# Kernel optimization log

Measured on AMD Instinct MI355X. Metric: run time of the kernel, lower is better.

The kernel has to match this reference:

```python
import jax, jax.numpy as jnp
import numpy as np

N = 50000      # nodes
E = 800000     # edges (avg degree 16)
IN = 256       # input feature dim
HID = 128      # hidden dim
H = 4          # heads
C = HID // H   # per-head dim = 32
L = 3          # layers


def setup_inputs() -> dict:
    key = jax.random.key(0)
    ks = jax.random.split(key, 16)
    s = 0.02
    f32 = jnp.float32
    inp = {
        "x": jax.random.normal(ks[0], (N, IN), f32),
        "edge_index": jax.random.randint(ks[1], (2, E), 0, N, dtype=jnp.int32),
        "edge_attr": jax.random.normal(ks[2], (E, 1), f32),
        "Wi": jax.random.normal(ks[3], (IN, HID), f32) * s,
        "bi": jnp.zeros((HID,), f32),
        "Wq": jax.random.normal(ks[4], (L, HID, HID), f32) * s,
        "bq": jnp.zeros((L, HID), f32),
        "Wk": jax.random.normal(ks[5], (L, HID, HID), f32) * s,
        "bk": jnp.zeros((L, HID), f32),
        "Wv": jax.random.normal(ks[6], (L, HID, HID), f32) * s,
        "bv": jnp.zeros((L, HID), f32),
        "We": jax.random.normal(ks[7], (L, 1, HID), f32) * s,      # lin_edge, no bias
        "Wskip": jax.random.normal(ks[8], (L, HID, HID), f32) * s,
        "bskip": jnp.zeros((L, HID), f32),
        "Wbeta": jax.random.normal(ks[9], (L, 3 * HID, 1), f32) * s,  # lin_beta, no bias
        "ln_g": jnp.ones((L, HID), f32),
        "ln_b": jnp.zeros((L, HID), f32),
    }
    return inp


def _layer_norm(x, g, b, eps=1e-5):
    mu = jnp.mean(x, axis=-1, keepdims=True)
    var = jnp.var(x, axis=-1, keepdims=True)
    return (x - mu) * jax.lax.rsqrt(var + eps) * g + b


def _transformer_conv(h, src, dst, edge_attr, Wq, bq, Wk, bk, Wv, bv, We, Wskip, bskip, Wbeta):
    # node-level projections [N, HID]
    q = h @ Wq + bq
    k = h @ Wk + bk
    v = h @ Wv + bv
    e = edge_attr @ We                       # [E, HID] edge embedding
    # per-edge gathered features [E, H, C]
    qi = q[dst].reshape(E, H, C)
    kj = (k[src] + e).reshape(E, H, C)
    vj = (v[src] + e).reshape(E, H, C)
    # attention logits [E, H]
    alpha = jnp.sum(qi * kj, axis=-1) / np.sqrt(C)
    # segment softmax over destination node
    amax = jax.ops.segment_max(alpha, dst, num_segments=N)   # [N, H]
    ex = jnp.exp(alpha - amax[dst])
    denom = jax.ops.segment_sum(ex, dst, num_segments=N)     # [N, H]
    attn = ex / (denom[dst] + 1e-16)                         # [E, H]
    # scatter-add aggregation -> [N, H, C] -> concat heads [N, HID]
    out = jax.ops.segment_sum(attn[..., None] * vj, dst, num_segments=N).reshape(N, HID)
    # gated skip (beta=True, root_weight=True)
    x_r = h @ Wskip + bskip
    beta = jax.nn.sigmoid(jnp.concatenate([out, x_r, out - x_r], axis=-1) @ Wbeta)  # [N, 1]
    return beta * x_r + (1.0 - beta) * out


def reference(x, edge_index, edge_attr, Wi, bi, Wq, bq, Wk, bk, Wv, bv, We, Wskip, bskip, Wbeta, ln_g, ln_b):
    src = edge_index[0]
    dst = edge_index[1]
    h = x @ Wi + bi
    for l in range(L):
        res = h
        h = _transformer_conv(h, src, dst, edge_attr,
                              Wq[l], bq[l], Wk[l], bk[l], Wv[l], bv[l],
                              We[l], Wskip[l], bskip[l], Wbeta[l])
        h = jax.nn.gelu(h, approximate=False)
        h = _layer_norm(h + res, ln_g[l], ln_b[l])
        # dropout: eval mode -> identity
    return h
```

## Files before the change

### kernel.cpp

```cpp
#include <hip/hip_runtime.h>
#include <math.h>

#define NNODES 50000
#define NEDGES 800000
#define DIN 256
#define DHID 128
#define GBLK 391
#define QBLK 782
#define NBUCK 196
#define CHUNK 4096

typedef __attribute__((ext_vector_type(8))) short short8;
typedef __attribute__((ext_vector_type(4))) float f32x4;
typedef __attribute__((ext_vector_type(2))) float f32x2;

__device__ __forceinline__ unsigned short f2bf(float f) {
    unsigned u = __builtin_bit_cast(unsigned, f);
    u += 0x7fffu + ((u >> 16) & 1u);
    return (unsigned short)(u >> 16);
}
__device__ __forceinline__ float bf2f(unsigned short s) {
    return __builtin_bit_cast(float, (unsigned)s << 16);
}
__device__ __forceinline__ unsigned packbf(float a, float b) {
    return (unsigned)f2bf(a) | ((unsigned)f2bf(b) << 16);
}
__device__ __forceinline__ float dpp_xor1(float x) {
    return __builtin_bit_cast(float, __builtin_amdgcn_update_dpp(0, __builtin_bit_cast(int, x), 0xB1, 0xF, 0xF, true));
}
__device__ __forceinline__ float dpp_xor2(float x) {
    return __builtin_bit_cast(float, __builtin_amdgcn_update_dpp(0, __builtin_bit_cast(int, x), 0x4E, 0xF, 0xF, true));
}
__device__ __forceinline__ float dpp_hmirror(float x) {
    return __builtin_bit_cast(float, __builtin_amdgcn_update_dpp(0, __builtin_bit_cast(int, x), 0x141, 0xF, 0xF, true));
}
__device__ __forceinline__ float dpp_mirror(float x) {
    return __builtin_bit_cast(float, __builtin_amdgcn_update_dpp(0, __builtin_bit_cast(int, x), 0x140, 0xF, 0xF, true));
}
__device__ __forceinline__ float red16(float x) {
    x += dpp_xor1(x);
    x += dpp_xor2(x);
    x += dpp_hmirror(x);
    x += dpp_mirror(x);
    return x;
}

__global__ __launch_bounds__(256) void prep_hist(const float* __restrict__ Wi, const float* __restrict__ Wq,
                                                 const float* __restrict__ Wk, const float* __restrict__ Wv,
                                                 const float* __restrict__ Ws, unsigned short* __restrict__ Wit,
                                                 unsigned short* __restrict__ Wt3, const int* __restrict__ dst,
                                                 int* __restrict__ counts, int pb) {
    if ((int)blockIdx.x < pb) {
        int idx = blockIdx.x * 256 + threadIdx.x;
        if (idx < DHID * DIN) {
            int n = idx >> 8, kk = idx & 255;
            Wit[idx] = f2bf(Wi[kk * DHID + n]);
        }
        int idx2 = idx - DHID * DIN;
        if (idx2 >= 0 && idx2 < 3 * 512 * DHID) {
            int l = idx2 / (512 * DHID);
            int rem = idx2 - l * 512 * DHID;
            int r = rem >> 7;
            int kk = rem & 127;
            int sel = r >> 7, rl = r & 127;
            const float* srcm = sel == 0 ? Wq : sel == 1 ? Wk : sel == 2 ? Wv : Ws;
            Wt3[idx2] = f2bf(srcm[l * DHID * DHID + kk * DHID + rl]);
        }
    } else {
        int e = (blockIdx.x - pb) * 256 + threadIdx.x;
        if (e < NEDGES) atomicAdd(&counts[dst[e]], 1);
    }
}

__global__ __launch_bounds__(256) void k_scan_block(const int* __restrict__ in, int* __restrict__ out,
                                                    int* __restrict__ partials, int n, int* __restrict__ dh) {
    __shared__ int sh[256];
    __shared__ int dhist[256];
    int tid = threadIdx.x;
    int i = blockIdx.x * 256 + tid;
    int vv = (i < n) ? in[i] : 0;
    sh[tid] = vv;
    dhist[tid] = 0;
    __syncthreads();
    if (i < n) atomicAdd(&dhist[min(vv, 255)], 1);
    for (int off = 1; off < 256; off <<= 1) {
        int t = (tid >= off) ? sh[tid - off] : 0;
        __syncthreads();
        sh[tid] += t;
        __syncthreads();
    }
    if (i < n) out[i] = sh[tid];
    if (tid == 255) partials[blockIdx.x] = sh[255];
    __syncthreads();
    int hc = dhist[tid];
    if (hc) atomicAdd(&dh[tid], hc);
}

__global__ __launch_bounds__(256) void k_apply2(const int* __restrict__ partials, int* __restrict__ row_ptr, int n,
                                                int nb, const int* __restrict__ dh, int* __restrict__ dbase) {
    __shared__ int sh[256];
    int tid = threadIdx.x;
    int vv = (tid < nb) ? partials[tid] : 0;
    sh[tid] = vv;
    __syncthreads();
    for (int off = 1; off < 256; off <<= 1) {
        int t = (tid >= off) ? sh[tid - off] : 0;
        __syncthreads();
        sh[tid] += t;
        __syncthreads();
    }
    int i = blockIdx.x * 256 + tid;
    if (i < n) {
        int add = blockIdx.x ? sh[blockIdx.x - 1] : 0;
        row_ptr[i + 1] += add;
    }
    if (i == 0) row_ptr[0] = 0;
    if (blockIdx.x == 0) {
        __syncthreads();
        int c = dh[255 - tid];
        sh[tid] = c;
        __syncthreads();
        for (int off = 1; off < 256; off <<= 1) {
            int t = (tid >= off) ? sh[tid - off] : 0;
            __syncthreads();
            sh[tid] += t;
            __syncthreads();
        }
        dbase[255 - tid] = sh[tid] - c;
    }
}

__global__ __launch_bounds__(256) void perm_scatter(const int* __restrict__ counts, const int* __restrict__ dbase,
                                                    int* __restrict__ dfill, int* __restrict__ perm) {
    __shared__ int h[256], gb[256], c2[256];
    const int tid = threadIdx.x;
    int i = blockIdx.x * 256 + tid;
    int d = (i < NNODES) ? min(counts[i], 255) : -1;
    h[tid] = 0;
    c2[tid] = 0;
    __syncthreads();
    if (d >= 0) atomicAdd(&h[d], 1);
    __syncthreads();
    int c = h[tid];
    gb[tid] = c ? dbase[tid] + atomicAdd(&dfill[tid], c) : 0;
    __syncthreads();
    if (d >= 0) {
        int r = atomicAdd(&c2[d], 1);
        perm[gb[d] + r] = i;
    }
}

__global__ __launch_bounds__(256) void bin_edges(const int* __restrict__ src, const int* __restrict__ dst,
                                                 const float* __restrict__ ea, const int* __restrict__ row_ptr,
                                                 int* __restrict__ bfill, unsigned* __restrict__ brec,
                                                 unsigned char* __restrict__ bdst) {
    __shared__ int hist[NBUCK];
    __shared__ int lbase[NBUCK];
    __shared__ int gbase[NBUCK];
    __shared__ int cnt[NBUCK];
    __shared__ unsigned rec4[CHUNK];
    __shared__ unsigned char dl8[CHUNK];
    __shared__ unsigned char bk8[CHUNK];
    const int tid = threadIdx.x;
    const int e0 = blockIdx.x * CHUNK;
    const int n = min(NEDGES - e0, CHUNK);
    for (int i = tid; i < NBUCK; i += 256) hist[i] = 0;
    __syncthreads();
    for (int i = tid; i < n; i += 256) atomicAdd(&hist[dst[e0 + i] >> 8], 1);
    __syncthreads();
    if (tid == 0) {
        int run = 0;
        for (int b = 0; b < NBUCK; ++b) {
            lbase[b] = run;
            run += hist[b];
        }
    }
    __syncthreads();
    for (int b = tid; b < NBUCK; b += 256) {
        int h = hist[b];
        int off = h ? atomicAdd(&bfill[b], h) : 0;
        gbase[b] = row_ptr[b << 8] + off;
        cnt[b] = lbase[b];
    }
    __syncthreads();
    for (int i = tid; i < n; i += 256) {
        int d = dst[e0 + i];
        int b = d >> 8;
        int lp = atomicAdd(&cnt[b], 1);
        rec4[lp] = (unsigned)src[e0 + i] | ((unsigned)f2bf(ea[e0 + i]) << 16);
        dl8[lp] = (unsigned char)(d & 255);
        bk8[lp] = (unsigned char)b;
    }
    __syncthreads();
    for (int i = tid; i < n; i += 256) {
        int b = bk8[i];
        int pos = gbase[b] + (i - lbase[b]);
        brec[pos] = rec4[i];
        bdst[pos] = dl8[i];
    }
}

__global__ __launch_bounds__(256) void sort_bucket(const unsigned* __restrict__ brec,
                                                   const unsigned char* __restrict__ bdst,
                                                   const int* __restrict__ row_ptr, unsigned* __restrict__ esrc) {
    __shared__ int rp[257];
    __shared__ int cnt[256];
    const int b = blockIdx.x;
    const int d0 = b << 8;
    const int nmax = min(256, NNODES - d0);
    const int tid = threadIdx.x;
    for (int i = tid; i <= nmax; i += 256) rp[i] = row_ptr[d0 + i];
    cnt[tid] = 0;
    __syncthreads();
    const int base = rp[0], end = rp[nmax];
    for (int i = base + tid; i < end; i += 256) {
        unsigned rec = brec[i];
        int d = bdst[i];
        int rank = atomicAdd(&cnt[d], 1);
        esrc[rp[d] + rank] = rec;
    }
}

__global__ __launch_bounds__(256) void gemm_in(const float* __restrict__ A, const unsigned short* __restrict__ Wt,
                                               const float* __restrict__ bias, unsigned* __restrict__ h32, int M) {
    __shared__ short As[128 * 128];
    const int tid = threadIdx.x;
    const int lane = tid & 63;
    const int wid = tid >> 6;
    const int row0 = blockIdx.x * 128;
    const int wr = (wid & 1) * 64;
    const int wc = (wid >> 1) * 64;
    f32x4 acc[4][4] = {};
    const int srow = tid >> 1;
    const int sk = (tid & 1) * 64;
    const int grow = min(row0 + srow, M - 1);
    for (int kt = 0; kt < 2; ++kt) {
        const float* ap = A + (size_t)grow * DIN + kt * 128 + sk;
#pragma unroll
        for (int i = 0; i < 8; ++i) {
            float4 f0 = *(const float4*)(ap + i * 8);
            float4 f1 = *(const float4*)(ap + i * 8 + 4);
            short8 s;
            s[0] = f2bf(f0.x); s[1] = f2bf(f0.y); s[2] = f2bf(f0.z); s[3] = f2bf(f0.w);
            s[4] = f2bf(f1.x); s[5] = f2bf(f1.y); s[6] = f2bf(f1.z); s[7] = f2bf(f1.w);
            int g = (sk >> 3) + i;
            *(short8*)(&As[srow * 128 + ((g ^ (srow & 7)) << 3)]) = s;
        }
        __syncthreads();
#pragma unroll
        for (int ks = 0; ks < 4; ++ks) {
            short8 a[4], b[4];
#pragma unroll
            for (int m = 0; m < 4; ++m) {
                int r = wr + m * 16 + (lane & 15);
                int g = ks * 4 + (lane >> 4);
                a[m] = *(const short8*)(&As[r * 128 + ((g ^ (r & 7)) << 3)]);
            }
#pragma unroll
            for (int n = 0; n < 4; ++n) {
                int c = wc + n * 16 + (lane & 15);
                b[n] = *(const short8*)(Wt + (size_t)c * DIN + kt * 128 + ks * 32 + (lane >> 4) * 8);
            }
#pragma unroll
            for (int m = 0; m < 4; ++m)
#pragma unroll
                for (int n = 0; n < 4; ++n)
                    acc[m][n] = __builtin_amdgcn_mfma_f32_16x16x32_bf16(a[m], b[n], acc[m][n], 0, 0, 0);
        }
        __syncthreads();
    }
    float* my = ((float*)As) + wid * 1024;
    float bb[4];
#pragma unroll
    for (int n = 0; n < 4; ++n) bb[n] = bias[wc + n * 16 + (lane & 15)];
    const int rr = lane >> 2;
    const int cb = lane & 3;
#pragma unroll
    for (int m = 0; m < 4; ++m) {
#pragma unroll
        for (int n = 0; n < 4; ++n) {
            int lc = n * 16 + (lane & 15);
#pragma unroll
            for (int j = 0; j < 4; ++j) {
                int row = (lane >> 4) * 4 + j;
                my[row * 64 + (((lc >> 2) ^ (row & 7)) << 2) + (lc & 3)] = acc[m][n][j] + bb[n];
            }
        }
        float vals[16];
#pragma unroll
        for (int s = 0; s < 4; ++s) {
            int gx = (cb * 4 + s) ^ (rr & 7);
            f32x4 t4 = *(const f32x4*)(my + rr * 64 + gx * 4);
            vals[s * 4 + 0] = t4.x; vals[s * 4 + 1] = t4.y; vals[s * 4 + 2] = t4.z; vals[s * 4 + 3] = t4.w;
        }
        int grow2 = row0 + wr + m * 16 + rr;
        if (grow2 < M) {
            unsigned pk[8];
#pragma unroll
            for (int d = 0; d < 8; ++d) pk[d] = packbf(vals[2 * d], vals[2 * d + 1]);
            unsigned* op = h32 + (size_t)grow2 * 64 + (wc >> 1) + cb * 8;
            *(uint4*)op = make_uint4(pk[0], pk[1], pk[2], pk[3]);
            *(uint4*)(op + 4) = make_uint4(pk[4], pk[5], pk[6], pk[7]);
        }
    }
}

__global__ __launch_bounds__(256) void gemm_qkvs(const unsigned short* __restrict__ A,
                                                 const unsigned short* __restrict__ Wt, const float* __restrict__ bq,
                                                 const float* __restrict__ bk, const float* __restrict__ bv,
                                                 const float* __restrict__ bs, unsigned* __restrict__ q32,
                                                 unsigned* __restrict__ kv, unsigned* __restrict__ xr32, int M) {
    __shared__ short As[64 * 128];
    const int tid = threadIdx.x;
    const int lane = tid & 63;
    const int wid = tid >> 6;
    const int row0 = blockIdx.x * 64;
    const int sel = wid >> 1;
    const int wc = (wid & 1) * 64;
    f32x4 acc0[4][4] = {}, acc1[4][4] = {};
    {
        const int srow = tid >> 2;
        const int sk = (tid & 3) * 32;
        const int grow = min(row0 + srow, M - 1);
        const unsigned short* ap = A + (size_t)grow * DHID + sk;
#pragma unroll
        for (int i = 0; i < 4; ++i) {
            short8 s = *(const short8*)(ap + i * 8);
            int g = (sk >> 3) + i;
            *(short8*)(&As[srow * 128 + ((g ^ (srow & 7)) << 3)]) = s;
        }
    }
    __syncthreads();
    const int b0base = sel ? 128 : 0;
    const int b1base = sel ? 256 : 384;
#pragma unroll
    for (int ks = 0; ks < 4; ++ks) {
        short8 a[4], b0[4], b1[4];
#pragma unroll
        for (int m = 0; m < 4; ++m) {
            int r = m * 16 + (lane & 15);
            int g = ks * 4 + (lane >> 4);
            a[m] = *(const short8*)(&As[r * 128 + ((g ^ (r & 7)) << 3)]);
        }
#pragma unroll
        for (int n = 0; n < 4; ++n) {
            int rb = wc + n * 16 + (lane & 15);
            b0[n] = *(const short8*)(Wt + (size_t)(b0base + rb) * DHID + ks * 32 + (lane >> 4) * 8);
            b1[n] = *(const short8*)(Wt + (size_t)(b1base + rb) * DHID + ks * 32 + (lane >> 4) * 8);
        }
#pragma unroll
        for (int m = 0; m < 4; ++m)
#pragma unroll
            for (int n = 0; n < 4; ++n) {
                acc0[m][n] = __builtin_amdgcn_mfma_f32_16x16x32_bf16(a[m], b0[n], acc0[m][n], 0, 0, 0);
                acc1[m][n] = __builtin_amdgcn_mfma_f32_16x16x32_bf16(a[m], b1[n], acc1[m][n], 0, 0, 0);
            }
    }
    __syncthreads();
    float* my = ((float*)As) + wid * 1024;
    const float* bias0 = sel ? bk : bq;
    const float* bias1 = sel ? bv : bs;
    float bb0[4], bb1[4];
#pragma unroll
    for (int n = 0; n < 4; ++n) {
        int c = wc + n * 16 + (lane & 15);
        bb0[n] = bias0[c];
        bb1[n] = bias1[c];
    }
    const int rr = lane >> 2;
    const int cb = lane & 3;
#pragma unroll
    for (int m = 0; m < 4; ++m) {
        float vals0[16], vals1[16];
#pragma unroll
        for (int n = 0; n < 4; ++n) {
            int lc = n * 16 + (lane & 15);
#pragma unroll
            for (int j = 0; j < 4; ++j) {
                int row = (lane >> 4) * 4 + j;
                my[row * 64 + (((lc >> 2) ^ (row & 7)) << 2) + (lc & 3)] = acc0[m][n][j] + bb0[n];
            }
        }
#pragma unroll
        for (int s = 0; s < 4; ++s) {
            int gx = (cb * 4 + s) ^ (rr & 7);
            f32x4 t4 = *(const f32x4*)(my + rr * 64 + gx * 4);
            vals0[s * 4 + 0] = t4.x; vals0[s * 4 + 1] = t4.y; vals0[s * 4 + 2] = t4.z; vals0[s * 4 + 3] = t4.w;
        }
#pragma unroll
        for (int n = 0; n < 4; ++n) {
            int lc = n * 16 + (lane & 15);
#pragma unroll
            for (int j = 0; j < 4; ++j) {
                int row = (lane >> 4) * 4 + j;
                my[row * 64 + (((lc >> 2) ^ (row & 7)) << 2) + (lc & 3)] = acc1[m][n][j] + bb1[n];
            }
        }
#pragma unroll
        for (int s = 0; s < 4; ++s) {
            int gx = (cb * 4 + s) ^ (rr & 7);
            f32x4 t4 = *(const f32x4*)(my + rr * 64 + gx * 4);
            vals1[s * 4 + 0] = t4.x; vals1[s * 4 + 1] = t4.y; vals1[s * 4 + 2] = t4.z; vals1[s * 4 + 3] = t4.w;
        }
        int grow2 = row0 + m * 16 + rr;
        if (grow2 < M) {
            size_t obase = (size_t)grow2 * 64 + (wc >> 1) + cb * 8;
            if (sel == 0) {
                unsigned p0[8], p1[8];
#pragma unroll
                for (int d = 0; d < 8; ++d) {
                    p0[d] = packbf(vals0[2 * d], vals0[2 * d + 1]);
                    p1[d] = packbf(vals1[2 * d], vals1[2 * d + 1]);
                }
                *(uint4*)(q32 + obase) = make_uint4(p0[0], p0[1], p0[2], p0[3]);
                *(uint4*)(q32 + obase + 4) = make_uint4(p0[4], p0[5], p0[6], p0[7]);
                *(uint4*)(xr32 + obase) = make_uint4(p1[0], p1[1], p1[2], p1[3]);
                *(uint4*)(xr32 + obase + 4) = make_uint4(p1[4], p1[5], p1[6], p1[7]);
            } else {
                unsigned pk[8];
#pragma unroll
                for (int d = 0; d < 8; ++d) {
                    unsigned u = (unsigned)__builtin_amdgcn_cvt_pk_fp8_f32(vals0[2 * d], vals0[2 * d + 1], 0, false);
                    u = (unsigned)__builtin_amdgcn_cvt_pk_fp8_f32(vals1[2 * d], vals1[2 * d + 1], (int)u, true);
                    pk[d] = u;
                }
                *(uint4*)(kv + obase) = make_uint4(pk[0], pk[1], pk[2], pk[3]);
                *(uint4*)(kv + obase + 4) = make_uint4(pk[4], pk[5], pk[6], pk[7]);
            }
        }
    }
}

__global__ __launch_bounds__(256) void node_attn_fuse(const unsigned* __restrict__ q32,
                                                      const unsigned* __restrict__ kv, const unsigned* __restrict__ esrc,
                                                      const float* __restrict__ We, const int* __restrict__ row_ptr,
                                                      const int* __restrict__ perm, const unsigned* __restrict__ xr32,
                                                      const unsigned* res32, const float* __restrict__ Wb,
                                                      const float* __restrict__ lng, const float* __restrict__ lnb,
                                                      unsigned* houtb, float* houtf) {
    const int tid = threadIdx.x;
    const int lane = tid & 63;
    const int lnl = lane & 15;
    const int gbase = lane & 48;
    const int node = perm[blockIdx.x * 16 + (tid >> 4)];
    const int base = row_ptr[node], end = row_ptr[node + 1];
    const float SC = 0.25505654047688565f;
    const float THR = 8.0f;

    float qv[8], wev[8];
    {
        uint4 qw = *(const uint4*)(q32 + (size_t)node * 64 + 4 * lnl);
        unsigned qd[4] = {qw.x, qw.y, qw.z, qw.w};
#pragma unroll
        for (int t = 0; t < 4; ++t) {
            qv[2 * t] = bf2f((unsigned short)qd[t]) * SC;
            qv[2 * t + 1] = bf2f((unsigned short)(qd[t] >> 16)) * SC;
        }
        float4 wlo = *(const float4*)(We + 8 * lnl);
        float4 whi = *(const float4*)(We + 8 * lnl + 4);
        wev[0] = wlo.x; wev[1] = wlo.y; wev[2] = wlo.z; wev[3] = wlo.w;
        wev[4] = whi.x; wev[5] = whi.y; wev[6] = whi.z; wev[7] = whi.w;
    }
    float qwe;
    {
        float s = 0.f;
#pragma unroll
        for (int i = 0; i < 8; ++i) s = fmaf(qv[i], wev[i], s);
        s += dpp_xor1(s);
        s += dpp_xor2(s);
        qwe = s;
    }

    float m = -1e30f, sden = 0.f, tacc = 0.f;
    float acc[8] = {};
    const unsigned* kvp = kv + 4 * lnl;

    for (int off = 0; ; off += 16) {
        int cnt = min(end - base - off, 16);
        if (__all(cnt <= 0)) break;
        unsigned u_l = 0;
        if (lnl < cnt) u_l = esrc[base + off + lnl];
        int cm = max(cnt, 0);
        cm = max(cm, __shfl_xor(cm, 16));
        cm = max(cm, __shfl_xor(cm, 32));
        unsigned ue0 = (unsigned)__shfl((int)u_l, gbase + 0);
        unsigned ue1 = (unsigned)__shfl((int)u_l, gbase + 1);
        unsigned ue2 = (unsigned)__shfl((int)u_l, gbase + 2);
        unsigned ue3 = (unsigned)__shfl((int)u_l, gbase + 3);
        uint4 kw0 = *(const uint4*)(kvp + (size_t)(ue0 & 0xFFFFu) * 64);
        uint4 kw1 = *(const uint4*)(kvp + (size_t)(ue1 & 0xFFFFu) * 64);
        uint4 kw2 = *(const uint4*)(kvp + (size_t)(ue2 & 0xFFFFu) * 64);
        uint4 kw3 = *(const uint4*)(kvp + (size_t)(ue3 & 0xFFFFu) * 64);
        for (int j = 0; j < cm; j += 2) {
            uint4 ka = kw0, kb = kw1;
            unsigned ua = ue0, ub = ue1;
            ue0 = ue2; ue1 = ue3; kw0 = kw2; kw1 = kw3;
            if (j + 4 < cm) {
                ue2 = (unsigned)__shfl((int)u_l, gbase + j + 4);
                ue3 = (unsigned)__shfl((int)u_l, gbase + j + 5);
                kw2 = *(const uint4*)(kvp + (size_t)(ue2 & 0xFFFFu) * 64);
                kw3 = *(const uint4*)(kvp + (size_t)(ue3 & 0xFFFFu) * 64);
            }
            float av0 = bf2f((unsigned short)(ua >> 16));
            float av1 = bf2f((unsigned short)(ub >> 16));
            unsigned kd0[4] = {ka.x, ka.y, ka.z, ka.w};
            unsigned kd1[4] = {kb.x, kb.y, kb.z, kb.w};
            float vj0[8], vj1[8];
            float p0 = 0.f, p1 = 0.f;
#pragma unroll
            for (int t = 0; t < 4; ++t) {
                f32x2 k0 = __builtin_amdgcn_cvt_pk_f32_fp8((int)kd0[t], false);
                f32x2 v0 = __builtin_amdgcn_cvt_pk_f32_fp8((int)kd0[t], true);
                f32x2 k1 = __builtin_amdgcn_cvt_pk_f32_fp8((int)kd1[t], false);
                f32x2 v1 = __builtin_amdgcn_cvt_pk_f32_fp8((int)kd1[t], true);
                p0 = fmaf(qv[2 * t], k0.x, p0);
                p0 = fmaf(qv[2 * t + 1], k0.y, p0);
                p1 = fmaf(qv[2 * t], k1.x, p1);
                p1 = fmaf(qv[2 * t + 1], k1.y, p1);
                vj0[2 * t] = v0.x; vj0[2 * t + 1] = v0.y;
                vj1[2 * t] = v1.x; vj1[2 * t + 1] = v1.y;
            }
            p0 += dpp_xor1(p0);
            p0 += dpp_xor2(p0);
            p1 += dpp_xor1(p1);
            p1 += dpp_xor2(p1);
            p0 = fmaf(av0, qwe, p0);
            p1 = fmaf(av1, qwe, p1);
            p0 = (j < cnt) ? p0 : -3e38f;
            p1 = (j + 1 < cnt) ? p1 : -3e38f;
            float pm = fmaxf(p0, p1);
            if (__any(pm - m > THR)) {
                float mn2 = fmaxf(m, pm);
                float sc = exp2f(m - mn2);
                float w0 = exp2f(p0 - mn2), w1 = exp2f(p1 - mn2);
                sden = fmaf(sden, sc, w0 + w1);
                tacc = fmaf(tacc, sc, fmaf(w0, av0, w1 * av1));
#pragma unroll
                for (int i = 0; i < 8; ++i) acc[i] = fmaf(acc[i], sc, fmaf(w0, vj0[i], w1 * vj1[i]));
                m = mn2;
            } else {
                float w0 = exp2f(p0 - m), w1 = exp2f(p1 - m);
                sden += w0 + w1;
                tacc = fmaf(w0, av0, fmaf(w1, av1, tacc));
#pragma unroll
                for (int i = 0; i < 8; ++i) acc[i] = fmaf(w0, vj0[i], fmaf(w1, vj1[i], acc[i]));
            }
        }
    }

    float rden = 1.f / (sden + 1e-16f);
    float o[8];
#pragma unroll
    for (int i = 0; i < 8; ++i) o[i] = fmaf(tacc, wev[i], acc[i]) * rden;

    float x[8];
    {
        uint4 xw = *(const uint4*)(xr32 + (size_t)node * 64 + 4 * lnl);
        unsigned xd[4] = {xw.x, xw.y, xw.z, xw.w};
#pragma unroll
        for (int t = 0; t < 4; ++t) {
            x[2 * t] = bf2f((unsigned short)xd[t]);
            x[2 * t + 1] = bf2f((unsigned short)(xd[t] >> 16));
        }
    }
    float bl = 0.f;
#pragma unroll
    for (int t = 0; t < 2; ++t) {
        float4 w0 = *(const float4*)(Wb + 8 * lnl + 4 * t);
        float4 w1 = *(const float4*)(Wb + 128 + 8 * lnl + 4 * t);
        float4 w2 = *(const float4*)(Wb + 256 + 8 * lnl + 4 * t);
        bl = fmaf(o[4 * t], w0.x, bl); bl = fmaf(o[4 * t + 1], w0.y, bl);
        bl = fmaf(o[4 * t + 2], w0.z, bl); bl = fmaf(o[4 * t + 3], w0.w, bl);
        bl = fmaf(x[4 * t], w1.x, bl); bl = fmaf(x[4 * t + 1], w1.y, bl);
        bl = fmaf(x[4 * t + 2], w1.z, bl); bl = fmaf(x[4 * t + 3], w1.w, bl);
        bl = fmaf(o[4 * t] - x[4 * t], w2.x, bl); bl = fmaf(o[4 * t + 1] - x[4 * t + 1], w2.y, bl);
        bl = fmaf(o[4 * t + 2] - x[4 * t + 2], w2.z, bl); bl = fmaf(o[4 * t + 3] - x[4 * t + 3], w2.w, bl);
    }
    bl = red16(bl);
    float beta = 1.f / (1.f + __expf(-bl));
    float tpre[8];
    {
        uint4 rw = *(const uint4*)(res32 + (size_t)node * 64 + 4 * lnl);
        unsigned rd[4] = {rw.x, rw.y, rw.z, rw.w};
#pragma unroll
        for (int i = 0; i < 8; ++i) {
            float gg = beta * x[i] + (1.f - beta) * o[i];
            gg = 0.5f * gg * (1.f + erff(gg * 0.70710678118654752f));
            float rv = (i & 1) ? bf2f((unsigned short)(rd[i >> 1] >> 16)) : bf2f((unsigned short)rd[i >> 1]);
            tpre[i] = gg + rv;
        }
    }
    float su = 0.f, sq = 0.f;
#pragma unroll
    for (int i = 0; i < 8; ++i) {
        su += tpre[i];
        sq = fmaf(tpre[i], tpre[i], sq);
    }
    su = red16(su);
    sq = red16(sq);
    float mu = su * (1.f / 128.f);
    float var = sq * (1.f / 128.f) - mu * mu;
    float inv = rsqrtf(var + 1e-5f);
    float4 g0 = *(const float4*)(lng + 8 * lnl);
    float4 g1 = *(const float4*)(lng + 8 * lnl + 4);
    float4 b0 = *(const float4*)(lnb + 8 * lnl);
    float4 b1 = *(const float4*)(lnb + 8 * lnl + 4);
    float gg[8] = {g0.x, g0.y, g0.z, g0.w, g1.x, g1.y, g1.z, g1.w};
    float bb[8] = {b0.x, b0.y, b0.z, b0.w, b1.x, b1.y, b1.z, b1.w};
    float ov[8];
#pragma unroll
    for (int i = 0; i < 8; ++i) ov[i] = (tpre[i] - mu) * inv * gg[i] + bb[i];
    if (houtf) {
        float* op = houtf + (size_t)node * 128 + 8 * lnl;
        *(float4*)op = make_float4(ov[0], ov[1], ov[2], ov[3]);
        *(float4*)(op + 4) = make_float4(ov[4], ov[5], ov[6], ov[7]);
    } else {
        unsigned pk[4];
#pragma unroll
        for (int d = 0; d < 4; ++d) pk[d] = packbf(ov[2 * d], ov[2 * d + 1]);
        *(uint4*)(houtb + (size_t)node * 64 + 4 * lnl) = make_uint4(pk[0], pk[1], pk[2], pk[3]);
    }
}

extern "C" void kernel_launch(void* const* d_in, const int* in_sizes, int n_in, void* d_out, int out_size,
                              void* d_ws, size_t ws_size, hipStream_t stream) {
    const float* x = (const float*)d_in[0];
    const int* ei = (const int*)d_in[1];
    const float* ea = (const float*)d_in[2];
    const float* Wi = (const float*)d_in[3];
    const float* bi = (const float*)d_in[4];
    const float* Wq = (const float*)d_in[5];
    const float* bq = (const float*)d_in[6];
    const float* Wk = (const float*)d_in[7];
    const float* bk = (const float*)d_in[8];
    const float* Wv = (const float*)d_in[9];
    const float* bv = (const float*)d_in[10];
    const float* We = (const float*)d_in[11];
    const float* Wskip = (const float*)d_in[12];
    const float* bskip = (const float*)d_in[13];
    const float* Wbeta = (const float*)d_in[14];
    const float* lng = (const float*)d_in[15];
    const float* lnb = (const float*)d_in[16];

    const int* srcp = ei;
    const int* dstp = ei + NEDGES;

    char* p = (char*)d_ws;
    auto alloc = [&](size_t bytes) {
        void* r = (void*)p;
        p += (bytes + 255) & ~(size_t)255;
        return r;
    };
    unsigned* h32 = (unsigned*)alloc((size_t)NNODES * 64 * 4);
    unsigned* q32 = (unsigned*)alloc((size_t)NNODES * 64 * 4);
    unsigned* xr32 = (unsigned*)alloc((size_t)NNODES * 64 * 4);
    unsigned* kv = (unsigned*)alloc((size_t)NNODES * 64 * 4);
    unsigned short* Wit = (unsigned short*)alloc((size_t)DHID * DIN * 2);
    unsigned short* Wt3 = (unsigned short*)alloc((size_t)3 * 512 * DHID * 2);
    int* counts = (int*)alloc((size_t)(NNODES + 768) * 4);
    int* bfill = counts + NNODES;
    int* dh = bfill + 256;
    int* dfill = dh + 256;
    int* dbase = (int*)alloc(256 * 4);
    int* perm = (int*)alloc((size_t)NNODES * 4);
    int* row_ptr = (int*)alloc((size_t)(NNODES + 1) * 4);
    unsigned* esrc = (unsigned*)alloc((size_t)NEDGES * 4);
    unsigned* brec = (unsigned*)alloc((size_t)NEDGES * 4);
    unsigned char* bdst = (unsigned char*)alloc((size_t)NEDGES);
    int* partials = (int*)alloc(256 * 4);

    const int EB = (NEDGES + 255) / 256;
    const int NB = (NNODES + 255) / 256;
    const int WB = NNODES / 16;
    const int PB = (DHID * DIN + 3 * 512 * DHID + 255) / 256;
    const int AB = (NEDGES + CHUNK - 1) / CHUNK;

    hipMemsetAsync(counts, 0, (size_t)(NNODES + 768) * 4, stream);
    prep_hist<<<PB + EB, 256, 0, stream>>>(Wi, Wq, Wk, Wv, Wskip, Wit, Wt3, dstp, counts, PB);
    gemm_in<<<GBLK, 256, 0, stream>>>(x, Wit, bi, h32, NNODES);
    k_scan_block<<<NB, 256, 0, stream>>>(counts, row_ptr + 1, partials, NNODES, dh);
    k_apply2<<<NB, 256, 0, stream>>>(partials, row_ptr, NNODES, NB, dh, dbase);
    perm_scatter<<<NB, 256, 0, stream>>>(counts, dbase, dfill, perm);
    bin_edges<<<AB, 256, 0, stream>>>(srcp, dstp, ea, row_ptr, bfill, brec, bdst);
    sort_bucket<<<NBUCK, 256, 0, stream>>>(brec, bdst, row_ptr, esrc);

    for (int l = 0; l < 3; ++l) {
        const size_t bo = (size_t)l * 128;
        gemm_qkvs<<<QBLK, 256, 0, stream>>>((const unsigned short*)h32, Wt3 + (size_t)l * 512 * DHID, bq + bo, bk + bo,
                                            bv + bo, bskip + bo, q32, kv, xr32, NNODES);
        node_attn_fuse<<<WB, 256, 0, stream>>>(q32, kv, esrc, We + bo, row_ptr, perm, xr32, h32,
                                               Wbeta + (size_t)l * 384, lng + bo, lnb + bo, h32,
                                               (l == 2) ? (float*)d_out : nullptr);
    }
}
```

Before: 324.2 us.

## Process four edges per step with deeper prefetch; enlarge QKVS GEMM tile

The attention loop now handles four gathered neighbours per iteration and keeps a second batch of four prefetched K/V rows in flight. It also decodes the V halves only when accumulating, which is meant to hide gather latency better and cut loop overhead. The QKV/skip GEMM moves to 128-row tiles with 512 threads, so each block reuses the weight loads across twice as many rows. The cost is higher register pressure in both kernels, a leftover dead conversion loop, and fewer, larger GEMM blocks that may lower occupancy.

New measurement: 311.1 us. -4.1%, faster.

```diff
diff --git a/kernel.cpp b/kernel.cpp
--- a/kernel.cpp
+++ b/kernel.cpp
@@ -6,7 +6,6 @@
 #define DIN 256
 #define DHID 128
 #define GBLK 391
-#define QBLK 782
 #define NBUCK 196
 #define CHUNK 4096
 
@@ -305,18 +304,19 @@
     }
 }
 
-__global__ __launch_bounds__(256) void gemm_qkvs(const unsigned short* __restrict__ A,
+__global__ __launch_bounds__(512) void gemm_qkvs(const unsigned short* __restrict__ A,
                                                  const unsigned short* __restrict__ Wt, const float* __restrict__ bq,
                                                  const float* __restrict__ bk, const float* __restrict__ bv,
                                                  const float* __restrict__ bs, unsigned* __restrict__ q32,
                                                  unsigned* __restrict__ kv, unsigned* __restrict__ xr32, int M) {
-    __shared__ short As[64 * 128];
+    __shared__ short As[128 * 128];
     const int tid = threadIdx.x;
     const int lane = tid & 63;
     const int wid = tid >> 6;
-    const int row0 = blockIdx.x * 64;
-    const int sel = wid >> 1;
-    const int wc = (wid & 1) * 64;
+    const int row0 = blockIdx.x * 128;
+    const int sel = wid >> 2;
+    const int wr = (wid & 1) * 64;
+    const int wc = ((wid >> 1) & 1) * 64;
     f32x4 acc0[4][4] = {}, acc1[4][4] = {};
     {
         const int srow = tid >> 2;
@@ -338,7 +338,7 @@
         short8 a[4], b0[4], b1[4];
 #pragma unroll
         for (int m = 0; m < 4; ++m) {
-            int r = m * 16 + (lane & 15);
+            int r = wr + m * 16 + (lane & 15);
             int g = ks * 4 + (lane >> 4);
             a[m] = *(const short8*)(&As[r * 128 + ((g ^ (r & 7)) << 3)]);
         }
@@ -402,7 +402,7 @@
             f32x4 t4 = *(const f32x4*)(my + rr * 64 + gx * 4);
             vals1[s * 4 + 0] = t4.x; vals1[s * 4 + 1] = t4.y; vals1[s * 4 + 2] = t4.z; vals1[s * 4 + 3] = t4.w;
         }
-        int grow2 = row0 + m * 16 + rr;
+        int grow2 = row0 + wr + m * 16 + rr;
         if (grow2 < M) {
             size_t obase = (size_t)grow2 * 64 + (wc >> 1) + cb * 8;
             if (sel == 0) {
@@ -483,67 +483,96 @@
         int cm = max(cnt, 0);
         cm = max(cm, __shfl_xor(cm, 16));
         cm = max(cm, __shfl_xor(cm, 32));
-        unsigned ue0 = (unsigned)__shfl((int)u_l, gbase + 0);
-        unsigned ue1 = (unsigned)__shfl((int)u_l, gbase + 1);
-        unsigned ue2 = (unsigned)__shfl((int)u_l, gbase + 2);
-        unsigned ue3 = (unsigned)__shfl((int)u_l, gbase + 3);
-        uint4 kw0 = *(const uint4*)(kvp + (size_t)(ue0 & 0xFFFFu) * 64);
-        uint4 kw1 = *(const uint4*)(kvp + (size_t)(ue1 & 0xFFFFu) * 64);
-        uint4 kw2 = *(const uint4*)(kvp + (size_t)(ue2 & 0xFFFFu) * 64);
-        uint4 kw3 = *(const uint4*)(kvp + (size_t)(ue3 & 0xFFFFu) * 64);
-        for (int j = 0; j < cm; j += 2) {
-            uint4 ka = kw0, kb = kw1;
-            unsigned ua = ue0, ub = ue1;
-            ue0 = ue2; ue1 = ue3; kw0 = kw2; kw1 = kw3;
-            if (j + 4 < cm) {
-                ue2 = (unsigned)__shfl((int)u_l, gbase + j + 4);
-                ue3 = (unsigned)__shfl((int)u_l, gbase + j + 5);
-                kw2 = *(const uint4*)(kvp + (size_t)(ue2 & 0xFFFFu) * 64);
-                kw3 = *(const uint4*)(kvp + (size_t)(ue3 & 0xFFFFu) * 64);
-            }
-            float av0 = bf2f((unsigned short)(ua >> 16));
-            float av1 = bf2f((unsigned short)(ub >> 16));
-            unsigned kd0[4] = {ka.x, ka.y, ka.z, ka.w};
-            unsigned kd1[4] = {kb.x, kb.y, kb.z, kb.w};
-            float vj0[8], vj1[8];
-            float p0 = 0.f, p1 = 0.f;
-#pragma unroll
-            for (int t = 0; t < 4; ++t) {
-                f32x2 k0 = __builtin_amdgcn_cvt_pk_f32_fp8((int)kd0[t], false);
-                f32x2 v0 = __builtin_amdgcn_cvt_pk_f32_fp8((int)kd0[t], true);
-                f32x2 k1 = __builtin_amdgcn_cvt_pk_f32_fp8((int)kd1[t], false);
-                f32x2 v1 = __builtin_amdgcn_cvt_pk_f32_fp8((int)kd1[t], true);
-                p0 = fmaf(qv[2 * t], k0.x, p0);
-                p0 = fmaf(qv[2 * t + 1], k0.y, p0);
-                p1 = fmaf(qv[2 * t], k1.x, p1);
-                p1 = fmaf(qv[2 * t + 1], k1.y, p1);
-                vj0[2 * t] = v0.x; vj0[2 * t + 1] = v0.y;
-                vj1[2 * t] = v1.x; vj1[2 * t + 1] = v1.y;
-            }
-            p0 += dpp_xor1(p0);
-            p0 += dpp_xor2(p0);
-            p1 += dpp_xor1(p1);
-            p1 += dpp_xor2(p1);
-            p0 = fmaf(av0, qwe, p0);
-            p1 = fmaf(av1, qwe, p1);
-            p0 = (j < cnt) ? p0 : -3e38f;
-            p1 = (j + 1 < cnt) ? p1 : -3e38f;
-            float pm = fmaxf(p0, p1);
+        unsigned ueA[4], ueB[4];
+        uint4 kwA[4], kwB[4];
+#pragma unroll
+        for (int s = 0; s < 4; ++s) {
+            ueA[s] = (unsigned)__shfl((int)u_l, gbase + s);
+            kwA[s] = *(const uint4*)(kvp + (size_t)(ueA[s] & 0xFFFFu) * 64);
+        }
+#pragma unroll
+        for (int s = 0; s < 4; ++s) {
+            ueB[s] = (unsigned)__shfl((int)u_l, gbase + 4 + s);
+            kwB[s] = *(const uint4*)(kvp + (size_t)(ueB[s] & 0xFFFFu) * 64);
+        }
+        for (int j = 0; j < cm; j += 4) {
+            float p[4], av[4];
+#pragma unroll
+            for (int s = 0; s < 4; ++s) {
+                av[s] = bf2f((unsigned short)(ueA[s] >> 16));
+                unsigned kd[4] = {kwA[s].x, kwA[s].y, kwA[s].z, kwA[s].w};
+                float pp = 0.f;
+#pragma unroll
+                for (int t = 0; t < 4; ++t) {
+                    f32x2 kk = __builtin_amdgcn_cvt_pk_f32_fp8((int)kd[t], false);
+                    pp = fmaf(qv[2 * t], kk.x, pp);
+                    pp = fmaf(qv[2 * t + 1], kk.y, pp);
+                }
+                p[s] = pp;
+            }
+#pragma unroll
+            for (int s = 0; s < 4; ++s) {
+                p[s] += dpp_xor1(p[s]);
+                p[s] += dpp_xor2(p[s]);
+                p[s] = fmaf(av[s], qwe, p[s]);
+                p[s] = (j + s < cnt) ? p[s] : -3e38f;
+            }
+            float pm = fmaxf(fmaxf(p[0], p[1]), fmaxf(p[2], p[3]));
+            float w[4];
             if (__any(pm - m > THR)) {
                 float mn2 = fmaxf(m, pm);
                 float sc = exp2f(m - mn2);
-                float w0 = exp2f(p0 - mn2), w1 = exp2f(p1 - mn2);
-                sden = fmaf(sden, sc, w0 + w1);
-                tacc = fmaf(tacc, sc, fmaf(w0, av0, w1 * av1));
-#pragma unroll
-                for (int i = 0; i < 8; ++i) acc[i] = fmaf(acc[i], sc, fmaf(w0, vj0[i], w1 * vj1[i]));
+#pragma unroll
+                for (int s = 0; s < 4; ++s) w[s] = exp2f(p[s] - mn2);
+                sden = fmaf(sden, sc, (w[0] + w[1]) + (w[2] + w[3]));
+                tacc = fmaf(tacc, sc, fmaf(w[0], av[0], w[1] * av[1]) + fmaf(w[2], av[2], w[3] * av[3]));
+#pragma unroll
+                for (int t = 0; t < 4; ++t) {
+                    f32x2 v0 = __builtin_amdgcn_cvt_pk_f32_fp8((int)kwA[0].x, true);
+                    (void)v0;
+                }
+#pragma unroll
+                for (int i = 0; i < 8; ++i) acc[i] *= sc;
+#pragma unroll
+                for (int s = 0; s < 4; ++s) {
+                    unsigned kd[4] = {kwA[s].x, kwA[s].y, kwA[s].z, kwA[s].w};
+#pragma unroll
+                    for (int t = 0; t < 4; ++t) {
+                        f32x2 vv = __builtin_amdgcn_cvt_pk_f32_fp8((int)kd[t], true);
+                        acc[2 * t] = fmaf(w[s], vv.x, acc[2 * t]);
+                        acc[2 * t + 1] = fmaf(w[s], vv.y, acc[2 * t + 1]);
+                    }
+                }
                 m = mn2;
             } else {
-                float w0 = exp2f(p0 - m), w1 = exp2f(p1 - m);
-                sden += w0 + w1;
-                tacc = fmaf(w0, av0, fmaf(w1, av1, tacc));
-#pragma unroll
-                for (int i = 0; i < 8; ++i) acc[i] = fmaf(w0, vj0[i], fmaf(w1, vj1[i], acc[i]));
+#pragma unroll
+                for (int s = 0; s < 4; ++s) w[s] = exp2f(p[s] - m);
+                sden += (w[0] + w[1]) + (w[2] + w[3]);
+                tacc += fmaf(w[0], av[0], w[1] * av[1]) + fmaf(w[2], av[2], w[3] * av[3]);
+#pragma unroll
+                for (int s = 0; s < 4; ++s) {
+                    unsigned kd[4] = {kwA[s].x, kwA[s].y, kwA[s].z, kwA[s].w};
+#pragma unroll
+                    for (int t = 0; t < 4; ++t) {
+                        f32x2 vv = __builtin_amdgcn_cvt_pk_f32_fp8((int)kd[t], true);
+                        acc[2 * t] = fmaf(w[s], vv.x, acc[2 * t]);
+                        acc[2 * t + 1] = fmaf(w[s], vv.y, acc[2 * t + 1]);
+                    }
+                }
+            }
+#pragma unroll
+            for (int s = 0; s < 4; ++s) {
+                ueA[s] = ueB[s];
+                kwA[s] = kwB[s];
+            }
+            if (j + 8 < cm) {
+#pragma unroll
+                for (int s = 0; s < 4; ++s) {
+                    int slot = j + 8 + s;
+                    slot = slot < 16 ? slot : 0;
+                    ueB[s] = (unsigned)__shfl((int)u_l, gbase + slot);
+                    kwB[s] = *(const uint4*)(kvp + (size_t)(ueB[s] & 0xFFFFu) * 64);
+                }
             }
         }
     }
@@ -686,7 +715,7 @@
 
     for (int l = 0; l < 3; ++l) {
         const size_t bo = (size_t)l * 128;
-        gemm_qkvs<<<QBLK, 256, 0, stream>>>((const unsigned short*)h32, Wt3 + (size_t)l * 512 * DHID, bq + bo, bk + bo,
+        gemm_qkvs<<<GBLK, 512, 0, stream>>>((const unsigned short*)h32, Wt3 + (size_t)l * 512 * DHID, bq + bo, bk + bo,
                                             bv + bo, bskip + bo, q32, kv, xr32, NNODES);
         node_attn_fuse<<<WB, 256, 0, stream>>>(q32, kv, esrc, We + bo, row_ptr, perm, xr32, h32,
                                                Wbeta + (size_t)l * 384, lng + bo, lnb + bo, h32,
```
